# Performance work log

Measured on AMD Instinct MI355X. Metric: run time of the kernel, lower is better.

Reference implementation:

```python
import jax, jax.numpy as jnp
import numpy as np

B, T, C, H = 2, 2048, 1024, 16
HD = C // H  # 64
EPS = 1e-5


def _ln(x, g, b):
    mu = jnp.mean(x, axis=-1, keepdims=True)
    var = jnp.var(x, axis=-1, keepdims=True)
    return (x - mu) * jax.lax.rsqrt(var + EPS) * g + b


def setup_inputs() -> dict:
    key = jax.random.key(0)
    ks = jax.random.split(key, 8)
    s = lambda n: 1.0 / np.sqrt(n)
    return {
        "x": jax.random.normal(ks[0], (B, T, C), dtype=jnp.float32),
        "ln1_g": jnp.ones((C,), jnp.float32), "ln1_b": jnp.zeros((C,), jnp.float32),
        "ln2_g": jnp.ones((C,), jnp.float32), "ln2_b": jnp.zeros((C,), jnp.float32),
        "w_in": jax.random.normal(ks[1], (C, 3 * C), jnp.float32) * s(C),
        "b_in": jnp.zeros((3 * C,), jnp.float32),
        "w_out": jax.random.normal(ks[2], (C, C), jnp.float32) * s(C),
        "b_out": jnp.zeros((C,), jnp.float32),
        "w_fc": jax.random.normal(ks[3], (C, 4 * C), jnp.float32) * s(C),
        "b_fc": jnp.zeros((4 * C,), jnp.float32),
        "w_proj": jax.random.normal(ks[4], (4 * C, C), jnp.float32) * s(4 * C),
        "b_proj": jnp.zeros((C,), jnp.float32),
    }


def reference(x, ln1_g, ln1_b, ln2_g, ln2_b, w_in, b_in, w_out, b_out,
              w_fc, b_fc, w_proj, b_proj):
    # --- residual 1: x + attn(ln1(x)) ---
    h = _ln(x, ln1_g, ln1_b)
    qkv = h @ w_in + b_in                          # (B,T,3C)
    # reshape to (B,T,H,3*HD) then chunk per head (matches torch code exactly)
    qkv = qkv.reshape(B, T, H, 3 * HD).transpose(0, 2, 1, 3)  # (B,H,T,3*HD)
    q, k, v = jnp.split(qkv, 3, axis=-1)           # each (B,H,T,HD)
    att = jnp.einsum('bhqd,bhkd->bhqk', q, k) / np.sqrt(HD)
    causal = jnp.tril(jnp.ones((T, T), bool))
    att = jnp.where(causal, att, -jnp.inf)
    att = jax.nn.softmax(att, axis=-1)
    o = jnp.einsum('bhqk,bhkd->bhqd', att, v)      # (B,H,T,HD)
    o = o.transpose(0, 2, 1, 3).reshape(B, T, C)
    x1 = x + (o @ w_out + b_out)
    # --- ln2 applied to residual stream, then residual 2 on top of ln2 output ---
    y = _ln(x1, ln2_g, ln2_b)
    mlp = jax.nn.gelu(y @ w_fc + b_fc, approximate=False) @ w_proj + b_proj
    return y + mlp
```

## Files before the change

kernel.cpp:

```cpp
#include <hip/hip_runtime.h>
#include <hip/hip_bf16.h>
#include <math.h>

typedef __bf16 bf16;
typedef __bf16 bf16x8 __attribute__((ext_vector_type(8)));
typedef __bf16 bf16x4 __attribute__((ext_vector_type(4)));
typedef float floatx4 __attribute__((ext_vector_type(4)));
typedef int intx4 __attribute__((ext_vector_type(4)));

#define B_ 2
#define T_ 2048
#define C_ 1024
#define H_ 16
#define HD_ 64

__device__ __forceinline__ void gload_lds16(const bf16* g, bf16* l) {
    __builtin_amdgcn_global_load_lds(
        (const __attribute__((address_space(1))) unsigned int*)(g),
        (__attribute__((address_space(3))) unsigned int*)(l), 16, 0, 0);
}

__global__ __launch_bounds__(256) void transpose_all(
        const float* __restrict__ w_in, const float* __restrict__ w_out,
        const float* __restrict__ w_fc, const float* __restrict__ w_proj,
        bf16* __restrict__ o_in, bf16* __restrict__ o_out,
        bf16* __restrict__ o_fc, bf16* __restrict__ o_proj) {
    __shared__ float shf[32 * 33];
    int t = blockIdx.x;
    int tid = threadIdx.x;
    const float* src; bf16* dst; int K, N, idx;
    if (t < 3072)      { src = w_in;   dst = o_in;   K = 1024; N = 3072; idx = t; }
    else if (t < 7168) { src = w_fc;   dst = o_fc;   K = 1024; N = 4096; idx = t - 3072; }
    else if (t < 8192) { src = w_out;  dst = o_out;  K = 1024; N = 1024; idx = t - 7168; }
    else               { src = w_proj; dst = o_proj; K = 4096; N = 1024; idx = t - 8192; }
    int ntx = N >> 5;
    int nt = (idx % ntx) * 32, kt = (idx / ntx) * 32;
    int tx = tid & 31, ty = tid >> 5;
    #pragma unroll
    for (int i = 0; i < 32; i += 8)
        shf[(ty + i) * 33 + tx] = src[(size_t)(kt + ty + i) * N + nt + tx];
    __syncthreads();
    #pragma unroll
    for (int i = 0; i < 32; i += 8)
        dst[(size_t)(nt + ty + i) * K + kt + tx] = (bf16)shf[tx * 33 + ty + i];
}

__global__ __launch_bounds__(256) void ln_kernel(const float* __restrict__ x,
                                                 const float* __restrict__ g,
                                                 const float* __restrict__ b,
                                                 bf16* __restrict__ out_b,
                                                 float* __restrict__ out_f) {
    int row = blockIdx.x;
    int tid = threadIdx.x;
    const float* xr = x + (size_t)row * C_;
    float4 v = ((const float4*)xr)[tid];
    float s  = v.x + v.y + v.z + v.w;
    float ss = v.x * v.x + v.y * v.y + v.z * v.z + v.w * v.w;
    #pragma unroll
    for (int off = 32; off; off >>= 1) {
        s  += __shfl_down(s, off);
        ss += __shfl_down(ss, off);
    }
    __shared__ float red[8];
    int wid = tid >> 6;
    if ((tid & 63) == 0) { red[wid] = s; red[wid + 4] = ss; }
    __syncthreads();
    s  = red[0] + red[1] + red[2] + red[3];
    ss = red[4] + red[5] + red[6] + red[7];
    float mean = s * (1.0f / C_);
    float var  = ss * (1.0f / C_) - mean * mean;
    float rstd = rsqrtf(var + 1e-5f);
    float4 gv = ((const float4*)g)[tid];
    float4 bv = ((const float4*)b)[tid];
    float o0 = (v.x - mean) * rstd * gv.x + bv.x;
    float o1 = (v.y - mean) * rstd * gv.y + bv.y;
    float o2 = (v.z - mean) * rstd * gv.z + bv.z;
    float o3 = (v.w - mean) * rstd * gv.w + bv.w;
    bf16x4 ob = { (bf16)o0, (bf16)o1, (bf16)o2, (bf16)o3 };
    ((bf16x4*)out_b)[(size_t)row * 256 + tid] = ob;
    if (out_f) {
        float4 of; of.x = o0; of.y = o1; of.z = o2; of.w = o3;
        ((float4*)out_f)[(size_t)row * 256 + tid] = of;
    }
}

__device__ __forceinline__ float gelu_fast(float x) {
    float z2 = 1.5957691216f * (x + 0.044715f * x * x * x);
    float e = __expf(z2);
    float t = 1.0f - 2.0f * __builtin_amdgcn_rcpf(e + 1.0f);
    return 0.5f * x * (1.0f + t);
}

#define BAR() do { __builtin_amdgcn_sched_barrier(0); __builtin_amdgcn_s_barrier(); __builtin_amdgcn_sched_barrier(0); } while (0)
#define VMC6() asm volatile("s_waitcnt vmcnt(6)" ::: "memory")
#define VMC0() asm volatile("s_waitcnt vmcnt(0)" ::: "memory")

#define LOAD_A(AS, QM) \
  { _Pragma("unroll") for (int i_ = 0; i_ < 4; i_++) { \
      const int r_ = wm128 + ((QM) * 4 + i_) * 16 + lm; \
      _Pragma("unroll") for (int kc_ = 0; kc_ < 2; kc_++) \
        aR[i_][kc_] = *(const bf16x8*)((AS) + r_ * 64 + ((((kc_ << 2) | quad) ^ (lm & 7)) << 3)); } }

#define LOAD_B(BS, QN) \
  { _Pragma("unroll") for (int j_ = 0; j_ < 2; j_++) { \
      const int r_ = wn64 + ((QN) * 2 + j_) * 16 + lm; \
      _Pragma("unroll") for (int kc_ = 0; kc_ < 2; kc_++) \
        bR[QN][j_][kc_] = *(const bf16x8*)((BS) + r_ * 64 + ((((kc_ << 2) | quad) ^ (lm & 7)) << 3)); } }

#define MFMA_Q(QM, QN) \
  { __builtin_amdgcn_s_setprio(1); \
    _Pragma("unroll") for (int i_ = 0; i_ < 4; i_++) \
    _Pragma("unroll") for (int j_ = 0; j_ < 2; j_++) \
    _Pragma("unroll") for (int kc_ = 0; kc_ < 2; kc_++) \
      acc[(QM) * 4 + i_][(QN) * 2 + j_] = __builtin_amdgcn_mfma_f32_16x16x32_bf16( \
          aR[i_][kc_], bR[QN][j_][kc_], acc[(QM) * 4 + i_][(QN) * 2 + j_], 0, 0, 0); \
    __builtin_amdgcn_s_setprio(0); }

#define STG(gb, lb, r0v, k0v) \
    gload_lds16((gb) + (size_t)((r0v) + sr8) * K + (k0v) + scb, (lb) + ((r0v) + wid * 8) * 64)

template<int MODE>
__global__ __launch_bounds__(512, 2) void gemm256(const bf16* __restrict__ A,
                                                  const bf16* __restrict__ Bt,
                                                  const float* __restrict__ bias,
                                                  void* __restrict__ out,
                                                  int M, int N, int K) {
    (void)M;
    __shared__ __align__(16) bf16 smem[4 * 256 * 64];
    bf16* As0 = smem;
    bf16* Bs0 = smem + 1 * 256 * 64;
    bf16* As1 = smem + 2 * 256 * 64;
    bf16* Bs1 = smem + 3 * 256 * 64;

    int ntn = N >> 8;
    int lin = blockIdx.x;
    int id  = (lin & 7) * (gridDim.x >> 3) + (lin >> 3);
    int mt = id / ntn, nt = id - mt * ntn;
    int m0 = mt << 8, n0 = nt << 8;

    int tid = threadIdx.x;
    int wid = __builtin_amdgcn_readfirstlane(tid >> 6);
    int lane = tid & 63;
    int lm = lane & 15, quad = lane >> 4;
    int wm128 = (wid & 1) * 128;
    int wn64  = (wid >> 1) * 64;

    const bf16* Ablk = A  + (size_t)m0 * K;
    const bf16* Bblk = Bt + (size_t)n0 * K;

    int sr8 = wid * 8 + (lane >> 3);
    int scb = ((lane & 7) ^ (lane >> 3)) << 3;

    floatx4 acc[8][4];
    #pragma unroll
    for (int f = 0; f < 8; f++)
        #pragma unroll
        for (int g = 0; g < 4; g++) { floatx4 z = {0.f, 0.f, 0.f, 0.f}; acc[f][g] = z; }
    bf16x8 aR[4][2], bR[2][2][2];

    int nI = K >> 7;

    STG(Ablk, As0, 0, 0);   STG(Ablk, As0, 64, 0);
    STG(Ablk, As0, 128, 0); STG(Ablk, As0, 192, 0);
    STG(Bblk, Bs0, 0, 0);   STG(Bblk, Bs0, 64, 0);
    STG(Bblk, Bs0, 128, 0); STG(Bblk, Bs0, 192, 0);
    STG(Ablk, As1, 0, 64);  STG(Ablk, As1, 128, 64);
    STG(Bblk, Bs1, 0, 64);  STG(Bblk, Bs1, 64, 64);
    STG(Ablk, As1, 64, 64); STG(Ablk, As1, 192, 64);
    VMC6();
    BAR();

    for (int it = 0; it < nI; it++) {
        int kE = (2 * it + 2) << 6;
        int kO = (2 * it + 3) << 6;
        int kT = (2 * it + 1) << 6;
        bool nl = (it + 1 < nI);
        LOAD_A(As0, 0); LOAD_B(Bs0, 0);
        STG(Bblk, Bs1, 128, kT); STG(Bblk, Bs1, 192, kT);
        BAR(); MFMA_Q(0, 0); BAR();
        LOAD_B(Bs0, 1);
        if (nl) { STG(Ablk, As0, 0, kE); STG(Ablk, As0, 128, kE); }
        BAR(); MFMA_Q(0, 1); BAR();
        LOAD_A(As0, 1);
        if (nl) { STG(Bblk, Bs0, 0, kE); STG(Bblk, Bs0, 64, kE); }
        BAR(); MFMA_Q(1, 0); BAR();
        if (nl) { STG(Ablk, As0, 64, kE); STG(Ablk, As0, 192, kE); }
        BAR(); MFMA_Q(1, 1);
        if (nl) { VMC6(); } else { VMC0(); }
        BAR();
        LOAD_A(As1, 0); LOAD_B(Bs1, 0);
        if (nl) { STG(Bblk, Bs0, 128, kE); STG(Bblk, Bs0, 192, kE); }
        BAR(); MFMA_Q(0, 0); BAR();
        LOAD_B(Bs1, 1);
        if (nl) { STG(Ablk, As1, 0, kO); STG(Ablk, As1, 128, kO); }
        BAR(); MFMA_Q(0, 1); BAR();
        LOAD_A(As1, 1);
        if (nl) { STG(Bblk, Bs1, 0, kO); STG(Bblk, Bs1, 64, kO); }
        BAR(); MFMA_Q(1, 0); BAR();
        if (nl) { STG(Ablk, As1, 64, kO); STG(Ablk, As1, 192, kO); }
        BAR(); MFMA_Q(1, 1);
        if (nl) { VMC6(); }
        BAR();
    }

    if (MODE == 0) {
        bf16* ob = (bf16*)out;
        #pragma unroll
        for (int f = 0; f < 8; f++) {
            int row0 = m0 + wm128 + f * 16 + quad * 4;
            #pragma unroll
            for (int g = 0; g < 4; g++) {
                int n = n0 + wn64 + g * 16 + lm;
                float bsn = bias[n];
                #pragma unroll
                for (int r = 0; r < 4; r++)
                    ob[(size_t)(row0 + r) * N + n] = (bf16)(acc[f][g][r] + bsn);
            }
        }
    } else {
        bf16* ob = (bf16*)out;
        bf16* patch = smem + wid * (64 * 68);
        #pragma unroll
        for (int h = 0; h < 2; h++) {
            #pragma unroll
            for (int ff = 0; ff < 4; ff++)
                #pragma unroll
                for (int g = 0; g < 4; g++) {
                    int n = n0 + wn64 + g * 16 + lm;
                    float bsn = bias[n];
                    #pragma unroll
                    for (int r = 0; r < 4; r++)
                        patch[(ff * 16 + quad * 4 + r) * 68 + g * 16 + lm] =
                            (bf16)gelu_fast(acc[h * 4 + ff][g][r] + bsn);
                }
            #pragma unroll
            for (int ff = 0; ff < 4; ff++)
                #pragma unroll
                for (int kc = 0; kc < 2; kc++) {
                    bf16x8 v = *(const bf16x8*)&patch[(ff * 16 + lm) * 68 + kc * 32 + quad * 8];
                    size_t row = (size_t)(m0 + wm128 + h * 64 + ff * 16 + lm);
                    *(bf16x8*)(ob + row * N + n0 + wn64 + kc * 32 + quad * 8) = v;
                }
        }
    }
}

#define VMCP(n) asm volatile("s_waitcnt vmcnt(" #n ")" ::: "memory")

#define STGP(kt) { bf16* bs_ = smem + ((kt) & 3) * 16384; \
    gload_lds16(Ab + (size_t)sr8 * K + (kt) * 64 + scb,        bs_ + (wid * 8) * 64); \
    gload_lds16(Ab + (size_t)(64 + sr8) * K + (kt) * 64 + scb, bs_ + (64 + wid * 8) * 64); \
    gload_lds16(Bb + (size_t)sr8 * K + (kt) * 64 + scb,        bs_ + 8192 + (wid * 8) * 64); \
    gload_lds16(Bb + (size_t)(64 + sr8) * K + (kt) * 64 + scb, bs_ + 8192 + (64 + wid * 8) * 64); }

__global__ __launch_bounds__(512, 2) void gemm_npipe(const bf16* __restrict__ A,
                                                     const bf16* __restrict__ Bt,
                                                     const float* __restrict__ bias,
                                                     const float* __restrict__ add,
                                                     float* __restrict__ out,
                                                     int N, int K) {
    __shared__ __align__(16) bf16 smem[4 * 16384];
    int lin = blockIdx.x;
    int xcd = lin & 7, loc = lin >> 3;
    int m0 = (xcd * 4 + (loc & 3)) * 128;
    int n0 = (loc >> 2) * 128;
    int tid = threadIdx.x;
    int wid = __builtin_amdgcn_readfirstlane(tid >> 6);
    int lane = tid & 63;
    int lm = lane & 15, quad = lane >> 4;
    int wm32 = (wid & 3) * 32, wn64 = (wid >> 2) * 64;
    int sr8 = wid * 8 + (lane >> 3);
    int scb = ((lane & 7) ^ (lane >> 3)) << 3;
    const bf16* Ab = A  + (size_t)m0 * K;
    const bf16* Bb = Bt + (size_t)n0 * K;
    int NT = K >> 6;

    floatx4 acc[2][4];
    #pragma unroll
    for (int i = 0; i < 2; i++)
        #pragma unroll
        for (int j = 0; j < 4; j++) { floatx4 z = {0.f, 0.f, 0.f, 0.f}; acc[i][j] = z; }
    bf16x8 aR[2][2], bR[4][2];

    STGP(0); STGP(1); STGP(2);
    VMCP(8);
    BAR();

    for (int t = 0; t < NT; t++) {
        if (t + 3 < NT) STGP(t + 3);
        bf16* bs = smem + (t & 3) * 16384;
        #pragma unroll
        for (int i = 0; i < 2; i++)
            #pragma unroll
            for (int kc = 0; kc < 2; kc++)
                aR[i][kc] = *(const bf16x8*)(bs + (wm32 + i * 16 + lm) * 64 +
                                             ((((kc << 2) | quad) ^ (lm & 7)) << 3));
        #pragma unroll
        for (int j = 0; j < 4; j++)
            #pragma unroll
            for (int kc = 0; kc < 2; kc++)
                bR[j][kc] = *(const bf16x8*)(bs + 8192 + (wn64 + j * 16 + lm) * 64 +
                                             ((((kc << 2) | quad) ^ (lm & 7)) << 3));
        __builtin_amdgcn_s_setprio(1);
        #pragma unroll
        for (int kc = 0; kc < 2; kc++)
            #pragma unroll
            for (int i = 0; i < 2; i++)
                #pragma unroll
                for (int j = 0; j < 4; j++)
                    acc[i][j] = __builtin_amdgcn_mfma_f32_16x16x32_bf16(
                        aR[i][kc], bR[j][kc], acc[i][j], 0, 0, 0);
        __builtin_amdgcn_s_setprio(0);
        if (t + 3 < NT)      { VMCP(8); }
        else if (t == NT - 3){ VMCP(4); }
        else if (t == NT - 2){ VMCP(0); }
        BAR();
    }

    #pragma unroll
    for (int i = 0; i < 2; i++)
        #pragma unroll
        for (int j = 0; j < 4; j++) {
            int mbase = m0 + wm32 + i * 16 + quad * 4;
            int n     = n0 + wn64 + j * 16 + lm;
            float bsn = bias[n];
            #pragma unroll
            for (int r = 0; r < 4; r++) {
                size_t idx = (size_t)(mbase + r) * N + n;
                out[idx] = acc[i][j][r] + bsn + add[idx];
            }
        }
}

#define QT_ 128
#define KT_ 64

__device__ __forceinline__ void vt_stage(bf16* VtB, bf16x8 vv, int vdb,
                                         int vcolb, int oddf) {
    intx4 vi = *(intx4*)&vv;
    intx4 pi;
    #pragma unroll
    for (int m = 0; m < 4; m++) pi[m] = __shfl_xor(vi[m], 8);
    #pragma unroll
    for (int j = 0; j < 4; j++) {
        int w0 = j >> 1, sh = (j & 1) * 16;
        unsigned int oe = ((unsigned int)vi[w0] >> sh) & 0xffffu;
        unsigned int pe = ((unsigned int)pi[w0] >> sh) & 0xffffu;
        unsigned int oo = ((unsigned int)vi[2 + w0] >> sh) & 0xffffu;
        unsigned int po = ((unsigned int)pi[2 + w0] >> sh) & 0xffffu;
        unsigned int de = oe | (pe << 16);
        unsigned int dn = po | (oo << 16);
        unsigned int dw = oddf ? dn : de;
        *(unsigned int*)(VtB + (size_t)(vdb + j) * 72 + vcolb) = dw;
    }
}

__global__ __launch_bounds__(512) void attn_mfma_kernel(const bf16* __restrict__ qkv,
                                                        bf16* __restrict__ Opart,
                                                        float* __restrict__ mlw) {
    int bh = blockIdx.x;
    int b = bh >> 4, h = bh & 15;
    int cy = blockIdx.y;
    int y, ci;
    if (cy < 4)       { y = cy;                   ci = 0; }
    else if (cy < 12) { y = 4 + ((cy - 4) >> 1);  ci = (cy - 4) & 1; }
    else if (cy < 24) { y = 8 + (cy - 12) / 3;    ci = (cy - 12) % 3; }
    else              { y = 12 + ((cy - 24) >> 2); ci = (cy - 24) & 3; }
    int q0 = y * QT_;
    int tb = ci * 8;
    int te = 2 * y + 2; if (te > tb + 8) te = tb + 8;

    int tid = threadIdx.x;
    int wid = __builtin_amdgcn_readfirstlane(tid >> 6);
    int lane = tid & 63;
    int lm = lane & 15, quad = lane >> 4;
    int sw = lm & 7;
    int r0 = q0 + wid * 16;

    const bf16* base = qkv + (size_t)b * T_ * (3 * C_) + h * (3 * HD_);

    __shared__ __align__(16) bf16 Ks[2][KT_][64];
    __shared__ __align__(16) bf16 Vt[2][HD_][72];
    __shared__ __align__(16) bf16 PsT[8][16][64];

    bf16x8 qf[2];
    #pragma unroll
    for (int kc = 0; kc < 2; kc++) {
        bf16x8 t = *(const bf16x8*)(base + (size_t)(r0 + lm) * (3 * C_) + kc * 32 + quad * 8);
        #pragma unroll
        for (int e = 0; e < 8; e++) t[e] = (bf16)((float)t[e] * 0.1803368801f);
        qf[kc] = t;
    }

    floatx4 acc_o[4];
    #pragma unroll
    for (int dn = 0; dn < 4; dn++) { floatx4 z = {0.f, 0.f, 0.f, 0.f}; acc_o[dn] = z; }
    float mst = -1e30f, lst = 0.0f;

    int srow = tid >> 3;
    int scb  = ((lane & 7) ^ (lane >> 3)) << 3;
    int scol = (tid & 7) * 8;
    int oddf = srow & 1;
    int vcolb = (((srow >> 3) ^ (tid & 7)) << 3) + (srow & 6);
    int vdb   = scol + (oddf ? 4 : 0);

    {
        size_t gr = (size_t)(tb * KT_ + srow) * (3 * C_);
        gload_lds16(base + gr + HD_ + scb, &Ks[0][wid * 8][0]);
        bf16x8 vv = *(const bf16x8*)(base + gr + 2 * HD_ + scol);
        vt_stage(&Vt[0][0][0], vv, vdb, vcolb, oddf);
        __syncthreads();
    }

    for (int t = tb; t < te; t++) {
        int cur = t & 1;
        bool pre = (t + 1 < te);
        bf16x8 vv;
        if (pre) {
            size_t nrow = (size_t)((t + 1) * KT_ + srow) * (3 * C_);
            gload_lds16(base + nrow + HD_ + scb, &Ks[cur ^ 1][wid * 8][0]);
            vv = *(const bf16x8*)(base + nrow + 2 * HD_ + scol);
        }
        __builtin_amdgcn_sched_barrier(0);

        int k0 = t * KT_;
        if (k0 <= r0 + 15) {
            floatx4 st[4];
            #pragma unroll
            for (int bn = 0; bn < 4; bn++) { floatx4 z = {0.f, 0.f, 0.f, 0.f}; st[bn] = z; }
            #pragma unroll
            for (int kc = 0; kc < 2; kc++) {
                bf16x8 kf[4];
                #pragma unroll
                for (int bn = 0; bn < 4; bn++)
                    kf[bn] = *(const bf16x8*)(&Ks[cur][bn * 16 + lm]
                                              [((((kc << 2) | quad) ^ sw) << 3)]);
                __builtin_amdgcn_s_setprio(1);
                #pragma unroll
                for (int bn = 0; bn < 4; bn++)
                    st[bn] = __builtin_amdgcn_mfma_f32_16x16x32_bf16(kf[bn], qf[kc], st[bn], 0, 0, 0);
                __builtin_amdgcn_s_setprio(0);
            }

            float vv_[4][4];
            float rm = -1e30f;
            if (k0 + KT_ - 1 > r0) {
                int gq = r0 + lm;
                #pragma unroll
                for (int bn = 0; bn < 4; bn++) {
                    #pragma unroll
                    for (int r = 0; r < 4; r++) {
                        int key = k0 + bn * 16 + quad * 4 + r;
                        vv_[bn][r] = (key <= gq) ? st[bn][r] : -1e30f;
                    }
                    rm = fmaxf(rm, fmaxf(fmaxf(vv_[bn][0], vv_[bn][1]),
                                         fmaxf(vv_[bn][2], vv_[bn][3])));
                }
            } else {
                #pragma unroll
                for (int bn = 0; bn < 4; bn++) {
                    #pragma unroll
                    for (int r = 0; r < 4; r++) vv_[bn][r] = st[bn][r];
                    rm = fmaxf(rm, fmaxf(fmaxf(vv_[bn][0], vv_[bn][1]),
                                         fmaxf(vv_[bn][2], vv_[bn][3])));
                }
            }
            rm = fmaxf(rm, __shfl_xor(rm, 16));
            rm = fmaxf(rm, __shfl_xor(rm, 32));
            float mnew = fmaxf(mst, rm);
            float alpha = exp2f(mst - mnew);
            mst = mnew;
            float ps = 0.f;
            #pragma unroll
            for (int bn = 0; bn < 4; bn++) {
                float p0 = exp2f(vv_[bn][0] - mnew);
                float p1 = exp2f(vv_[bn][1] - mnew);
                float p2 = exp2f(vv_[bn][2] - mnew);
                float p3 = exp2f(vv_[bn][3] - mnew);
                ps += (p0 + p1) + (p2 + p3);
                bf16x4 pk = { (bf16)p0, (bf16)p1, (bf16)p2, (bf16)p3 };
                int kb = bn * 2 + (quad >> 1);
                int col = ((kb ^ sw) << 3) + (quad & 1) * 4;
                *(bf16x4*)(&PsT[wid][lm][col]) = pk;
            }
            ps += __shfl_xor(ps, 16);
            ps += __shfl_xor(ps, 32);
            lst = lst * alpha + ps;

            #pragma unroll
            for (int r = 0; r < 4; r++) {
                float ar = __shfl(alpha, quad * 4 + r);
                #pragma unroll
                for (int dn = 0; dn < 4; dn++) acc_o[dn][r] *= ar;
            }

            __asm__ volatile("s_waitcnt lgkmcnt(0)" ::: "memory");

            #pragma unroll
            for (int kc = 0; kc < 2; kc++) {
                bf16x8 pa = *(const bf16x8*)(&PsT[wid][lm][((kc * 4 + quad) ^ sw) << 3]);
                bf16x8 vfr[4];
                #pragma unroll
                for (int dn = 0; dn < 4; dn++) {
                    int d = dn * 16 + lm;
                    int swd = (d >> 3) & 7;
                    vfr[dn] = *(const bf16x8*)(&Vt[cur][d][(((kc * 4 + quad) ^ swd) << 3)]);
                }
                __builtin_amdgcn_s_setprio(1);
                #pragma unroll
                for (int dn = 0; dn < 4; dn++)
                    acc_o[dn] = __builtin_amdgcn_mfma_f32_16x16x32_bf16(pa, vfr[dn], acc_o[dn], 0, 0, 0);
                __builtin_amdgcn_s_setprio(0);
            }
        }

        if (pre) vt_stage(&Vt[cur ^ 1][0][0], vv, vdb, vcolb, oddf);
        __syncthreads();
    }

    #pragma unroll
    for (int r = 0; r < 4; r++) {
        #pragma unroll
        for (int dn = 0; dn < 4; dn++)
            PsT[wid][quad * 4 + r][dn * 16 + lm] = (bf16)acc_o[dn][r];
    }
    __asm__ volatile("s_waitcnt lgkmcnt(0)" ::: "memory");
    bf16* op = Opart + ((size_t)bh * 40 + cy) * (QT_ * HD_) + (wid * 16 + lm) * HD_;
    #pragma unroll
    for (int kcl = 0; kcl < 2; kcl++) {
        bf16x8 v = *(const bf16x8*)&PsT[wid][lm][kcl * 32 + quad * 8];
        *(bf16x8*)(op + kcl * 32 + quad * 8) = v;
    }
    if (lane < 16) {
        float* mlp = mlw + (((size_t)bh * 40 + cy) * QT_ + wid * 16 + lane) * 2;
        mlp[0] = mst;
        mlp[1] = lst;
    }
}

__global__ __launch_bounds__(256) void attn_combine(const bf16* __restrict__ Opart,
                                                    const float* __restrict__ mlw,
                                                    bf16* __restrict__ ob) {
    int bh = blockIdx.x, y = blockIdx.y;
    int b = bh >> 4, h = bh & 15;
    int nc = (y >> 2) + 1;
    int cy0 = (y < 4) ? y : (y < 8) ? (4 + ((y - 4) << 1))
             : (y < 12) ? (12 + (y - 8) * 3) : (24 + ((y - 12) << 2));
    int tid = threadIdx.x;
    int row = tid >> 1, half = tid & 1;
    size_t cbase = (size_t)bh * 40 + cy0;
    const float* mlp = mlw + (cbase * QT_ + row) * 2;
    float m0 = mlp[0], l0 = mlp[1];
    float m1 = -1e30f, l1 = 0.f, m2 = -1e30f, l2 = 0.f, m3 = -1e30f, l3 = 0.f;
    if (nc > 1) { m1 = mlp[2 * QT_];     l1 = mlp[2 * QT_ + 1]; }
    if (nc > 2) { m2 = mlp[2 * 2 * QT_]; l2 = mlp[2 * 2 * QT_ + 1]; }
    if (nc > 3) { m3 = mlp[3 * 2 * QT_]; l3 = mlp[3 * 2 * QT_ + 1]; }
    float mx = fmaxf(fmaxf(m0, m1), fmaxf(m2, m3));
    float s0 = exp2f(m0 - mx), s1 = exp2f(m1 - mx);
    float s2 = exp2f(m2 - mx), s3 = exp2f(m3 - mx);
    float wsum = s0 * l0 + s1 * l1 + s2 * l2 + s3 * l3;

    const bf16* op = Opart + cbase * (QT_ * HD_) + row * HD_ + half * 32;
    float acc[32];
    #pragma unroll
    for (int v8 = 0; v8 < 4; v8++) {
        bf16x8 v = *(const bf16x8*)(op + v8 * 8);
        #pragma unroll
        for (int e = 0; e < 8; e++) acc[v8 * 8 + e] = s0 * (float)v[e];
    }
    if (nc > 1) {
        #pragma unroll
        for (int v8 = 0; v8 < 4; v8++) {
            bf16x8 v = *(const bf16x8*)(op + QT_ * HD_ + v8 * 8);
            #pragma unroll
            for (int e = 0; e < 8; e++) acc[v8 * 8 + e] += s1 * (float)v[e];
        }
    }
    if (nc > 2) {
        #pragma unroll
        for (int v8 = 0; v8 < 4; v8++) {
            bf16x8 v = *(const bf16x8*)(op + 2 * QT_ * HD_ + v8 * 8);
            #pragma unroll
            for (int e = 0; e < 8; e++) acc[v8 * 8 + e] += s2 * (float)v[e];
        }
    }
    if (nc > 3) {
        #pragma unroll
        for (int v8 = 0; v8 < 4; v8++) {
            bf16x8 v = *(const bf16x8*)(op + 3 * QT_ * HD_ + v8 * 8);
            #pragma unroll
            for (int e = 0; e < 8; e++) acc[v8 * 8 + e] += s3 * (float)v[e];
        }
    }
    float inv = 1.0f / wsum;
    bf16* dst = ob + ((size_t)(b * T_ + y * QT_ + row)) * C_ + h * HD_ + half * 32;
    #pragma unroll
    for (int v8 = 0; v8 < 4; v8++) {
        bf16x8 o;
        #pragma unroll
        for (int e = 0; e < 8; e++) o[e] = (bf16)(acc[v8 * 8 + e] * inv);
        *(bf16x8*)(dst + v8 * 8) = o;
    }
}

extern "C" void kernel_launch(void* const* d_in, const int* in_sizes, int n_in,
                              void* d_out, int out_size, void* d_ws, size_t ws_size,
                              hipStream_t stream) {
    (void)in_sizes; (void)n_in; (void)out_size; (void)ws_size;
    const float* x      = (const float*)d_in[0];
    const float* ln1_g  = (const float*)d_in[1];
    const float* ln1_b  = (const float*)d_in[2];
    const float* ln2_g  = (const float*)d_in[3];
    const float* ln2_b  = (const float*)d_in[4];
    const float* w_in   = (const float*)d_in[5];
    const float* b_in   = (const float*)d_in[6];
    const float* w_out  = (const float*)d_in[7];
    const float* b_out  = (const float*)d_in[8];
    const float* w_fc   = (const float*)d_in[9];
    const float* b_fc   = (const float*)d_in[10];
    const float* w_proj = (const float*)d_in[11];
    const float* b_proj = (const float*)d_in[12];

    char* ws = (char*)d_ws;
    const size_t MB = 1024 * 1024;
    bf16*  w_inT   = (bf16*)(ws + 0);
    bf16*  w_outT  = (bf16*)(ws + 6 * MB);
    bf16*  w_fcT   = (bf16*)(ws + 8 * MB);
    bf16*  w_projT = (bf16*)(ws + 16 * MB);
    bf16*  qkv     = (bf16*)(ws + 24 * MB);
    bf16*  fc_b    = (bf16*)(ws + 24 * MB);
    bf16*  o_b     = (bf16*)(ws + 56 * MB);
    bf16*  y_b     = (bf16*)(ws + 56 * MB);
    bf16*  h_b     = (bf16*)(ws + 64 * MB);
    float* x1      = (float*)(ws + 64 * MB);
    float* y_f     = (float*)(ws + 80 * MB);
    bf16*  Opart   = (bf16*)(ws + 64 * MB);
    float* mlw     = (float*)(ws + 84 * MB);

    const int M = B_ * T_;

    transpose_all<<<12288, 256, 0, stream>>>(w_in, w_out, w_fc, w_proj,
                                             w_inT, w_outT, w_fcT, w_projT);

    ln_kernel<<<M, 256, 0, stream>>>(x, ln1_g, ln1_b, h_b, nullptr);
    gemm256<0><<<(M >> 8) * ((3 * C_) >> 8), 512, 0, stream>>>(h_b, w_inT, b_in,
                                                               qkv, M, 3 * C_, C_);
    attn_mfma_kernel<<<dim3(B_ * H_, 40), 512, 0, stream>>>(qkv, Opart, mlw);
    attn_combine<<<dim3(B_ * H_, T_ / QT_), 256, 0, stream>>>(Opart, mlw, o_b);
    gemm_npipe<<<256, 512, 0, stream>>>(o_b, w_outT, b_out, x, x1, C_, C_);
    ln_kernel<<<M, 256, 0, stream>>>(x1, ln2_g, ln2_b, y_b, y_f);
    gemm256<1><<<(M >> 8) * ((4 * C_) >> 8), 512, 0, stream>>>(y_b, w_fcT, b_fc,
                                                               fc_b, M, 4 * C_, C_);
    gemm_npipe<<<256, 512, 0, stream>>>(fc_b, w_projT, b_proj, y_f,
                                        (float*)d_out, C_, 4 * C_);
}
```

Baseline: 329.5 us.

## Remap GEMM block-to-tile order per XCD and stage MODE 0 epilogue through LDS

The block-index-to-tile mapping in both GEMM kernels is rewritten so that the blocks on one XCD cover a compact 2D region of output tiles, meant to improve L2 reuse of A and B tiles within each XCD's private cache. The MODE 0 (QKV) epilogue now uses the same LDS patch transposition as the GELU path, writing coalesced 16-byte rows instead of scattered scalar bf16 stores. Loop variables are renamed to avoid shadowing the new mapping variables. The new mapping hardcodes the grid shapes (ntn==12 vs 16) and relies on specific tile counts.

```diff
diff --git a/kernel.cpp b/kernel.cpp
--- a/kernel.cpp
+++ b/kernel.cpp
@@ -134,8 +134,13 @@
 
     int ntn = N >> 8;
     int lin = blockIdx.x;
-    int id  = (lin & 7) * (gridDim.x >> 3) + (lin >> 3);
-    int mt = id / ntn, nt = id - mt * ntn;
+    int x = lin & 7, local = lin >> 3;
+    int RN = (ntn == 12) ? 3 : 4;
+    int rsz = 4 * RN;
+    int r = local / rsz, s = local - r * rsz;
+    int rid = x + 8 * r;
+    int mt = (rid & 3) * 4 + (s & 3);
+    int nt = (rid >> 2) * RN + (s >> 2);
     int m0 = mt << 8, n0 = nt << 8;
 
     int tid = threadIdx.x;
@@ -203,45 +208,31 @@
         BAR();
     }
 
-    if (MODE == 0) {
-        bf16* ob = (bf16*)out;
-        #pragma unroll
-        for (int f = 0; f < 8; f++) {
-            int row0 = m0 + wm128 + f * 16 + quad * 4;
+    bf16* ob = (bf16*)out;
+    bf16* patch = smem + wid * (64 * 68);
+    #pragma unroll
+    for (int h = 0; h < 2; h++) {
+        #pragma unroll
+        for (int ff = 0; ff < 4; ff++)
             #pragma unroll
             for (int g = 0; g < 4; g++) {
                 int n = n0 + wn64 + g * 16 + lm;
                 float bsn = bias[n];
                 #pragma unroll
-                for (int r = 0; r < 4; r++)
-                    ob[(size_t)(row0 + r) * N + n] = (bf16)(acc[f][g][r] + bsn);
-            }
-        }
-    } else {
-        bf16* ob = (bf16*)out;
-        bf16* patch = smem + wid * (64 * 68);
-        #pragma unroll
-        for (int h = 0; h < 2; h++) {
-            #pragma unroll
-            for (int ff = 0; ff < 4; ff++)
-                #pragma unroll
-                for (int g = 0; g < 4; g++) {
-                    int n = n0 + wn64 + g * 16 + lm;
-                    float bsn = bias[n];
-                    #pragma unroll
-                    for (int r = 0; r < 4; r++)
-                        patch[(ff * 16 + quad * 4 + r) * 68 + g * 16 + lm] =
-                            (bf16)gelu_fast(acc[h * 4 + ff][g][r] + bsn);
+                for (int r2 = 0; r2 < 4; r2++) {
+                    float v = acc[h * 4 + ff][g][r2] + bsn;
+                    if (MODE == 1) v = gelu_fast(v);
+                    patch[(ff * 16 + quad * 4 + r2) * 68 + g * 16 + lm] = (bf16)v;
                 }
-            #pragma unroll
-            for (int ff = 0; ff < 4; ff++)
-                #pragma unroll
-                for (int kc = 0; kc < 2; kc++) {
-                    bf16x8 v = *(const bf16x8*)&patch[(ff * 16 + lm) * 68 + kc * 32 + quad * 8];
-                    size_t row = (size_t)(m0 + wm128 + h * 64 + ff * 16 + lm);
-                    *(bf16x8*)(ob + row * N + n0 + wn64 + kc * 32 + quad * 8) = v;
-                }
-        }
+            }
+        #pragma unroll
+        for (int ff = 0; ff < 4; ff++)
+            #pragma unroll
+            for (int kc = 0; kc < 2; kc++) {
+                bf16x8 v = *(const bf16x8*)&patch[(ff * 16 + lm) * 68 + kc * 32 + quad * 8];
+                size_t row = (size_t)(m0 + wm128 + h * 64 + ff * 16 + lm);
+                *(bf16x8*)(ob + row * N + n0 + wn64 + kc * 32 + quad * 8) = v;
+            }
     }
 }
 
@@ -261,9 +252,11 @@
                                                      int N, int K) {
     __shared__ __align__(16) bf16 smem[4 * 16384];
     int lin = blockIdx.x;
-    int xcd = lin & 7, loc = lin >> 3;
-    int m0 = (xcd * 4 + (loc & 3)) * 128;
-    int n0 = (loc >> 2) * 128;
+    int x = lin & 7, local = lin >> 3;
+    int r = local >> 2, s = local & 3;
+    int rid = x + 8 * r;
+    int m0 = ((rid & 15) * 2 + (s & 1)) * 128;
+    int n0 = ((rid >> 4) * 2 + (s >> 1)) * 128;
     int tid = threadIdx.x;
     int wid = __builtin_amdgcn_readfirstlane(tid >> 6);
     int lane = tid & 63;
@@ -325,9 +318,9 @@
             int n     = n0 + wn64 + j * 16 + lm;
             float bsn = bias[n];
             #pragma unroll
-            for (int r = 0; r < 4; r++) {
-                size_t idx = (size_t)(mbase + r) * N + n;
-                out[idx] = acc[i][j][r] + bsn + add[idx];
+            for (int r2 = 0; r2 < 4; r2++) {
+                size_t idx = (size_t)(mbase + r2) * N + n;
+                out[idx] = acc[i][j][r2] + bsn + add[idx];
             }
         }
 }
@@ -449,9 +442,9 @@
                 #pragma unroll
                 for (int bn = 0; bn < 4; bn++) {
                     #pragma unroll
-                    for (int r = 0; r < 4; r++) {
-                        int key = k0 + bn * 16 + quad * 4 + r;
-                        vv_[bn][r] = (key <= gq) ? st[bn][r] : -1e30f;
+                    for (int r2 = 0; r2 < 4; r2++) {
+                        int key = k0 + bn * 16 + quad * 4 + r2;
+                        vv_[bn][r2] = (key <= gq) ? st[bn][r2] : -1e30f;
                     }
                     rm = fmaxf(rm, fmaxf(fmaxf(vv_[bn][0], vv_[bn][1]),
                                          fmaxf(vv_[bn][2], vv_[bn][3])));
@@ -460,7 +453,7 @@
                 #pragma unroll
                 for (int bn = 0; bn < 4; bn++) {
                     #pragma unroll
-                    for (int r = 0; r < 4; r++) vv_[bn][r] = st[bn][r];
+                    for (int r2 = 0; r2 < 4; r2++) vv_[bn][r2] = st[bn][r2];
                     rm = fmaxf(rm, fmaxf(fmaxf(vv_[bn][0], vv_[bn][1]),
                                          fmaxf(vv_[bn][2], vv_[bn][3])));
                 }
@@ -488,10 +481,10 @@
             lst = lst * alpha + ps;
 
             #pragma unroll
-            for (int r = 0; r < 4; r++) {
-                float ar = __shfl(alpha, quad * 4 + r);
-                #pragma unroll
-                for (int dn = 0; dn < 4; dn++) acc_o[dn][r] *= ar;
+            for (int r2 = 0; r2 < 4; r2++) {
+                float ar = __shfl(alpha, quad * 4 + r2);
+                #pragma unroll
+                for (int dn = 0; dn < 4; dn++) acc_o[dn][r2] *= ar;
             }
 
             __asm__ volatile("s_waitcnt lgkmcnt(0)" ::: "memory");
@@ -519,10 +512,10 @@
     }
 
     #pragma unroll
-    for (int r = 0; r < 4; r++) {
+    for (int r2 = 0; r2 < 4; r2++) {
         #pragma unroll
         for (int dn = 0; dn < 4; dn++)
-            PsT[wid][quad * 4 + r][dn * 16 + lm] = (bf16)acc_o[dn][r];
+            PsT[wid][quad * 4 + r2][dn * 16 + lm] = (bf16)acc_o[dn][r2];
     }
     __asm__ volatile("s_waitcnt lgkmcnt(0)" ::: "memory");
     bf16* op = Opart + ((size_t)bh * 40 + cy) * (QT_ * HD_) + (wid * 16 + lm) * HD_;
```

Measured after the change: 324.1 us. Within noise of the previous version (-1.7%).
